# Performance work log

Hardware: AMD Instinct MI355X
Metric: run time of the kernel (lower is better)

Reference implementation:

```python
import jax, jax.numpy as jnp
import numpy as np

NEG_INF = -1e9


def _gru_cell(x, h, W_ih, W_hh, b_ih, b_hh):
    # torch GRUCell math, gate order [r; z; n]
    gx = x @ W_ih.T + b_ih          # [B, 3H]
    gh = h @ W_hh.T + b_hh          # [B, 3H]
    xr, xz, xn = jnp.split(gx, 3, axis=-1)
    hr, hz, hn = jnp.split(gh, 3, axis=-1)
    r = jax.nn.sigmoid(xr + hr)
    z = jax.nn.sigmoid(xz + hz)
    n = jnp.tanh(xn + r * hn)
    return (1.0 - z) * n + z * h


def setup_inputs() -> dict:
    key = jax.random.key(0)
    ks = jax.random.split(key, 8)
    B, N, D, H, P = 64, 2048, 256, 256, 256
    s = 0.05
    return {
        "sequence": jax.random.normal(ks[0], (B, N, D), jnp.float32),
        "hidden_t": jax.random.normal(ks[1], (B, H), jnp.float32),
        "sequence_mask": jnp.ones((B, N), jnp.float32),
        "num_steps": 2,
        "W_seq": jax.random.normal(ks[2], (D, P), jnp.float32) * s,
        "W_h": jax.random.normal(ks[3], (H, P), jnp.float32) * s,
        "v_att": jax.random.normal(ks[4], (P,), jnp.float32) * s,
        "W_ih": jax.random.normal(ks[5], (3 * H, D), jnp.float32) * s,
        "W_hh": jax.random.normal(ks[6], (3 * H, H), jnp.float32) * s,
        "b_ih": jnp.zeros((3 * H,), jnp.float32),
        "b_hh": jnp.zeros((3 * H,), jnp.float32),
    }


def reference(sequence, hidden_t, sequence_mask, num_steps,
              W_seq, W_h, v_att, W_ih, W_hh, b_ih, b_hh):
    # Precompute the sequence projection once (invariant across decode steps).
    seq_proj = jnp.einsum("bnd,dp->bnp", sequence, W_seq)   # [B, N, P]
    mask_bias = jnp.where(sequence_mask > 0, 0.0, NEG_INF)  # [B, N]

    def step(h, _):
        # projection similarity: v . tanh(W1 s_i + W2 h)
        proj = jnp.tanh(seq_proj + (h @ W_h)[:, None, :])   # [B, N, P]
        scores = jnp.einsum("bnp,p->bn", proj, v_att) + mask_bias
        w = jax.nn.softmax(scores, axis=-1)                  # [B, N]
        vec = jnp.einsum("bn,bnd->bd", w, sequence)          # [B, D]
        h_new = _gru_cell(vec, h, W_ih, W_hh, b_ih, b_hh)
        return h_new, w

    _, ws = jax.lax.scan(step, hidden_t, None, length=num_steps)  # [T, B, N]
    return jnp.transpose(ws, (1, 0, 2))                            # [B, T, N]
```

## Files before the change

### kernel.cpp

```cpp
#include <hip/hip_runtime.h>
#include <cstdint>

using u16 = unsigned short;
using u32 = unsigned int;
typedef __attribute__((ext_vector_type(8))) short bf16x8;
typedef __attribute__((ext_vector_type(8))) u16 u16x8;
typedef __attribute__((ext_vector_type(16))) float f32x16;
typedef __attribute__((ext_vector_type(4))) u32 u32x4;

#define DEV static __device__ __forceinline__

DEV u16 bf16_rne(float x) {
  u32 u = __float_as_uint(x);
  u32 r = (u + 0x7FFFu + ((u >> 16) & 1u)) >> 16;
  return (u16)r;
}
DEV float bf16f(u16 h) { return __uint_as_float(((u32)h) << 16); }

DEV u32 cvt_pk_bf16(float lo, float hi) {
  u32 d;
  asm("v_cvt_pk_bf16_f32 %0, %1, %2" : "=v"(d) : "v"(lo), "v"(hi));
  return d;
}

DEV float fast_tanh(float x) {
  float e = __expf(2.0f * x);
  return 1.0f - 2.0f / (e + 1.0f);
}
DEV float sigmoidf_(float x) { return 1.0f / (1.0f + __expf(-x)); }

__global__ __launch_bounds__(256) void prep_w(const float* __restrict__ Wseq,
                                              const float* __restrict__ Wih,
                                              const float* __restrict__ Whh,
                                              u16* __restrict__ WfG,
                                              float* __restrict__ WT,
                                              float* __restrict__ UT) {
  const int bid = blockIdx.x, t = threadIdx.x;
  if (bid < 32) {
    const int unit = bid * 4 + (t >> 6);
    const int lane = t & 63, l31 = lane & 31, koct = lane >> 5;
    const int pt8 = unit >> 4, kt = unit & 15;
    u16x8 o;
#pragma unroll
    for (int e = 0; e < 8; ++e)
      o[e] = bf16_rne(
          Wseq[(long)(kt * 16 + koct * 8 + e) * 256 + pt8 * 32 + l31]);
    *(u16x8*)(WfG + (long)unit * 512 + lane * 8) = o;
  } else {
    const int gid = bid - 32;
    const float* src = (gid >= 12) ? Whh : Wih;
    float* dst = (gid >= 12) ? UT : WT;
    const int g = (gid % 12) * 64 + (t & 63);
    const int dq = t >> 6;
#pragma unroll 4
    for (int d = dq * 64; d < dq * 64 + 64; ++d)
      dst[(long)d * 768 + g] = src[(long)g * 256 + d];
  }
}

__global__ __launch_bounds__(256) void hw_q(const float* __restrict__ h,
                                            const float* __restrict__ Wh,
                                            float* __restrict__ hw) {
  const int q = blockIdx.x, b = blockIdx.y, t = threadIdx.x;
  __shared__ float sh[256];
  __shared__ float sP[4][64];
  sh[t] = h[b * 256 + t];
  __syncthreads();
  const int j4 = t & 63, dg = t >> 6;
  const int j = q * 64 + j4;
  float g = 0.f;
#pragma unroll 4
  for (int k = dg * 64; k < dg * 64 + 64; ++k)
    g = fmaf(sh[k], Wh[(long)k * 256 + j], g);
  sP[dg][j4] = g;
  __syncthreads();
  if (t < 64)
    hw[b * 256 + q * 64 + t] = (sP[0][t] + sP[1][t]) + (sP[2][t] + sP[3][t]);
}

struct EpiSmem {
  float sQ[64][5];
  float se[64];
  float shw[256];
  float svv[256];
};

DEV void epilogue(EpiSmem& sm, const f32x16& a00, const f32x16& a10,
                  const u16* bs, const float* __restrict__ mask,
                  float* __restrict__ wbuf, float* __restrict__ esum,
                  float* __restrict__ part, long nbase, int esumIdx,
                  long partBase, int t, int lane, int w, int l31, int koct,
                  int pg, int ng) {
  float sc0 = 0.f;
#pragma unroll
  for (int r = 0; r < 16; ++r) {
    const int pidx = pg * 64 + (r & 3) + 8 * (r >> 2) + 4 * koct;
    sc0 = fmaf(sm.svv[pidx], fast_tanh(a00[r] + sm.shw[pidx]), sc0);
  }
#pragma unroll
  for (int r = 0; r < 16; ++r) {
    const int pidx = pg * 64 + 32 + (r & 3) + 8 * (r >> 2) + 4 * koct;
    sc0 = fmaf(sm.svv[pidx], fast_tanh(a10[r] + sm.shw[pidx]), sc0);
  }
  sc0 += __shfl_xor(sc0, 32, 64);
  if (koct == 0) sm.sQ[ng * 32 + l31][pg] = sc0;
  __syncthreads();
  if (t < 64) {
    float s = (sm.sQ[t][0] + sm.sQ[t][1]) + (sm.sQ[t][2] + sm.sQ[t][3]);
    const long n = nbase + t;
    float e = (mask[n] > 0.f) ? __expf(s) : 0.f;
    sm.se[t] = e;
    wbuf[n] = e;
    float s4 = e;
#pragma unroll
    for (int off = 1; off < 64; off <<= 1) s4 += __shfl_xor(s4, off, 64);
    if (t == 0) esum[esumIdx] = s4;
  }
  __syncthreads();
#pragma unroll
  for (int kk = 0; kk < 2; ++kk) {
    const int kt = w + kk * 8;
    float vd0 = 0, vd1 = 0, vd2 = 0, vd3 = 0, vd4 = 0, vd5 = 0, vd6 = 0,
          vd7 = 0;
#pragma unroll
    for (int t8 = 0; t8 < 2; ++t8) {
      u16x8 q = *(const u16x8*)(bs + ((long)(t8 * 16 + kt) * 64 + lane) * 8);
      const float wv = sm.se[t8 * 32 + l31];
      vd0 = fmaf(wv, bf16f((u16)q[0]), vd0);
      vd1 = fmaf(wv, bf16f((u16)q[1]), vd1);
      vd2 = fmaf(wv, bf16f((u16)q[2]), vd2);
      vd3 = fmaf(wv, bf16f((u16)q[3]), vd3);
      vd4 = fmaf(wv, bf16f((u16)q[4]), vd4);
      vd5 = fmaf(wv, bf16f((u16)q[5]), vd5);
      vd6 = fmaf(wv, bf16f((u16)q[6]), vd6);
      vd7 = fmaf(wv, bf16f((u16)q[7]), vd7);
    }
#pragma unroll
    for (int off = 1; off < 32; off <<= 1) {
      vd0 += __shfl_xor(vd0, off, 64);
      vd1 += __shfl_xor(vd1, off, 64);
      vd2 += __shfl_xor(vd2, off, 64);
      vd3 += __shfl_xor(vd3, off, 64);
      vd4 += __shfl_xor(vd4, off, 64);
      vd5 += __shfl_xor(vd5, off, 64);
      vd6 += __shfl_xor(vd6, off, 64);
      vd7 += __shfl_xor(vd7, off, 64);
    }
    if (l31 == 0) {
      float4 o0 = {vd0, vd1, vd2, vd3};
      float4 o1 = {vd4, vd5, vd6, vd7};
      float* pp = part + partBase * 256 + kt * 16 + koct * 8;
      *(float4*)pp = o0;
      *(float4*)(pp + 4) = o1;
    }
  }
}

__global__ __launch_bounds__(512, 4) void step0k(
    const float* __restrict__ seq, u16* __restrict__ seqF,
    const u16* __restrict__ WfG, const float* __restrict__ hwbuf,
    const float* __restrict__ vatt, const float* __restrict__ mask,
    float* __restrict__ wbuf, float* __restrict__ esum,
    float* __restrict__ part, int N, int NCH, int B) {
  __shared__ __align__(16) u16 sR[16384];
  __shared__ EpiSmem sm;

  const int t = threadIdx.x, lane = t & 63, w = t >> 6;
  const int l31 = lane & 31, koct = lane >> 5;
  const int pg = w >> 1, ng = w & 1;
  const int b = blockIdx.y, ch = blockIdx.x;
  char* sRb = (char*)sR;
  const long chbase = (long)(b * NCH + ch) << 14;

  {
    const float* src = seq + ((long)b * N + ch * 64) * 256;
#pragma unroll
    for (int i = 0; i < 4; ++i) {
      const int idx = i * 4096 + t * 8;
      float4 x = *(const float4*)(src + idx);
      float4 y = *(const float4*)(src + idx + 4);
      u32x4 o;
      o[0] = cvt_pk_bf16(x.x, x.y);
      o[1] = cvt_pk_bf16(x.z, x.w);
      o[2] = cvt_pk_bf16(y.x, y.y);
      o[3] = cvt_pk_bf16(y.z, y.w);
      const int row = idx >> 8, colb = (idx & 255) * 2;
      *(u32x4*)(sRb + row * 512 + (colb ^ ((row & 31) << 4))) = o;
    }
  }
  if (t < 256) {
    sm.shw[t] = hwbuf[b * 256 + t];
    sm.svv[t] = vatt[t];
  }
  __syncthreads();

  {
    u16* dst = seqF + chbase;
#pragma unroll
    for (int i = 0; i < 4; ++i) {
      const int uidx = i * 512 + t;
      const int ln = uidx & 63, unit = uidx >> 6;
      const int kt = unit & 15, t8 = unit >> 4;
      const int row = t8 * 32 + (ln & 31);
      const int colb = (kt * 16 + (ln >> 5) * 8) * 2;
      u16x8 v = *(const u16x8*)(sRb + row * 512 + (colb ^ ((row & 31) << 4)));
      *(u16x8*)(dst + (long)uidx * 8) = v;
    }
  }

  f32x16 a00 = (f32x16)0.f, a10 = (f32x16)0.f;
  {
    const u16* wa0 = WfG + (long)pg * 16384 + lane * 8;
    const u16* wa1 = wa0 + 8192;
    const int row0 = ng * 32 + l31;
    const char* p0 = sRb + row0 * 512;
    const int sw0 = (row0 & 31) << 4;
    const int cb = koct * 16;
#pragma unroll 4
    for (int kt = 0; kt < 16; ++kt) {
      bf16x8 af0 = *(const bf16x8*)(wa0 + kt * 512);
      bf16x8 af1 = *(const bf16x8*)(wa1 + kt * 512);
      bf16x8 bf0 = *(const bf16x8*)(p0 + ((kt * 32 + cb) ^ sw0));
      a00 = __builtin_amdgcn_mfma_f32_32x32x16_bf16(af0, bf0, a00, 0, 0, 0);
      a10 = __builtin_amdgcn_mfma_f32_32x32x16_bf16(af1, bf0, a10, 0, 0, 0);
    }
  }
  __syncthreads();
  epilogue(sm, a00, a10, seqF + chbase, mask, wbuf, esum, part,
           (long)b * N + ch * 64, b * NCH + ch, (long)ch * B + b, t, lane, w,
           l31, koct, pg, ng);
}

__global__ __launch_bounds__(512, 4) void step1k(
    const u16* __restrict__ seqF, const u16* __restrict__ WfG,
    const float* __restrict__ hwbuf, const float* __restrict__ vatt,
    const float* __restrict__ mask, float* __restrict__ wbuf,
    float* __restrict__ esum, float* __restrict__ part, int N, int NCH,
    int B) {
  __shared__ EpiSmem sm;
  const int t = threadIdx.x, lane = t & 63, w = t >> 6;
  const int l31 = lane & 31, koct = lane >> 5;
  const int pg = w >> 1, ng = w & 1;
  const int b = blockIdx.y, ch = blockIdx.x;
  const long chbase = (long)(b * NCH + ch) << 14;

  if (t < 256) {
    sm.shw[t] = hwbuf[b * 256 + t];
    sm.svv[t] = vatt[t];
  }

  const u16* bs0 = seqF + chbase + ng * 8192 + lane * 8;
  const u16* wa0 = WfG + (long)pg * 16384 + lane * 8;
  const u16* wa1 = wa0 + 8192;

  f32x16 a00 = (f32x16)0.f, a10 = (f32x16)0.f;

  u16x8 A0c, A1c, B0c, A0n, A1n, B0n;
  A0c = *(const u16x8*)(wa0);
  A1c = *(const u16x8*)(wa1);
  B0c = *(const u16x8*)(bs0);

#define MFMA2(A0, A1, B0)                                                      \
  {                                                                            \
    bf16x8 af0 = *(bf16x8*)&A0, af1 = *(bf16x8*)&A1;                           \
    bf16x8 bf0 = *(bf16x8*)&B0;                                                \
    a00 = __builtin_amdgcn_mfma_f32_32x32x16_bf16(af0, bf0, a00, 0, 0, 0);     \
    a10 = __builtin_amdgcn_mfma_f32_32x32x16_bf16(af1, bf0, a10, 0, 0, 0);     \
  }

#pragma unroll
  for (int kt2 = 0; kt2 < 8; ++kt2) {
    const int kn = kt2 * 2 + 1;
    A0n = *(const u16x8*)(wa0 + kn * 512);
    A1n = *(const u16x8*)(wa1 + kn * 512);
    B0n = *(const u16x8*)(bs0 + kn * 512);
    MFMA2(A0c, A1c, B0c);
    if (kt2 < 7) {
      const int kc = kt2 * 2 + 2;
      A0c = *(const u16x8*)(wa0 + kc * 512);
      A1c = *(const u16x8*)(wa1 + kc * 512);
      B0c = *(const u16x8*)(bs0 + kc * 512);
    }
    MFMA2(A0n, A1n, B0n);
  }
#undef MFMA2

  __syncthreads();
  epilogue(sm, a00, a10, seqF + chbase, mask, wbuf, esum, part,
           (long)b * N + ch * 64, b * NCH + ch, (long)ch * B + b, t, lane, w,
           l31, koct, pg, ng);
}

__global__ __launch_bounds__(256) void finalize_gru(
    const float* __restrict__ part, const float* __restrict__ esumP, int ecnt,
    const float* __restrict__ hprev, const float* __restrict__ WT,
    const float* __restrict__ UT, const float* __restrict__ bih,
    const float* __restrict__ bhh, const float* __restrict__ wbuf,
    float* __restrict__ out, float* __restrict__ hnew, int N, int T, int step,
    int NP, int B) {
  const int q = blockIdx.x, b = blockIdx.y, t = threadIdx.x;
  __shared__ float sv[256], sh[256], sP[6][4][64];
  float S = 0.f;
  for (int i = 0; i < ecnt; ++i) S += esumP[b * ecnt + i];
  const float inv = 1.f / S;
  float a = 0.f;
  for (int cc = 0; cc < NP; ++cc) a += part[((long)cc * B + b) * 256 + t];
  sv[t] = a * inv;
  sh[t] = hprev[b * 256 + t];
  __syncthreads();
  const int j4 = t & 63, dg = t >> 6;
  const int j = q * 64 + j4;
  float g0 = 0, g1 = 0, g2 = 0, g3 = 0, g4 = 0, g5 = 0;
#pragma unroll 4
  for (int d = dg * 64; d < dg * 64 + 64; ++d) {
    const float vd = sv[d], hd = sh[d];
    const float* wr_ = WT + (long)d * 768 + j;
    const float* ur_ = UT + (long)d * 768 + j;
    g0 = fmaf(vd, wr_[0], g0);
    g1 = fmaf(vd, wr_[256], g1);
    g2 = fmaf(vd, wr_[512], g2);
    g3 = fmaf(hd, ur_[0], g3);
    g4 = fmaf(hd, ur_[256], g4);
    g5 = fmaf(hd, ur_[512], g5);
  }
  sP[0][dg][j4] = g0;
  sP[1][dg][j4] = g1;
  sP[2][dg][j4] = g2;
  sP[3][dg][j4] = g3;
  sP[4][dg][j4] = g4;
  sP[5][dg][j4] = g5;
  __syncthreads();
  if (t < 64) {
    const int jj = q * 64 + t;
    float xr = bih[jj], xz = bih[256 + jj], xn = bih[512 + jj];
    float hr = bhh[jj], hz = bhh[256 + jj], hn = bhh[512 + jj];
#pragma unroll
    for (int dgg = 0; dgg < 4; ++dgg) {
      xr += sP[0][dgg][t];
      xz += sP[1][dgg][t];
      xn += sP[2][dgg][t];
      hr += sP[3][dgg][t];
      hz += sP[4][dgg][t];
      hn += sP[5][dgg][t];
    }
    float rr = sigmoidf_(xr + hr);
    float zz = sigmoidf_(xz + hz);
    float nn = fast_tanh(xn + rr * hn);
    hnew[b * 256 + jj] = (1.f - zz) * nn + zz * sh[jj];
  }
  const long ob = ((long)b * T + step) * N;
  const int nq = N >> 2;
  for (int i = 0; i * 256 < nq; ++i) {
    const int n = q * nq + i * 256 + t;
    out[ob + n] = wbuf[(long)b * N + n] * inv;
  }
}

extern "C" void kernel_launch(void* const* d_in, const int* in_sizes, int n_in,
                              void* d_out, int out_size, void* d_ws,
                              size_t ws_size, hipStream_t stream) {
  (void)n_in;
  (void)ws_size;
  const float* seq = (const float*)d_in[0];
  const float* hidden = (const float*)d_in[1];
  const float* mask = (const float*)d_in[2];
  const float* Wseq = (const float*)d_in[4];
  const float* Wh = (const float*)d_in[5];
  const float* vatt = (const float*)d_in[6];
  const float* Wih = (const float*)d_in[7];
  const float* Whh = (const float*)d_in[8];
  const float* bih = (const float*)d_in[9];
  const float* bhh = (const float*)d_in[10];
  float* out = (float*)d_out;

  const int P = in_sizes[6];
  const int H = in_sizes[5] / P;
  const int B = in_sizes[1] / H;
  const int N = in_sizes[2] / B;
  const int T = out_size / (B * N);
  const long M = (long)B * N;
  const int NCH = N / 64;

  char* p = (char*)d_ws;
  auto alloc = [&](size_t bytes) {
    char* r = p;
    p += (bytes + 255) & ~(size_t)255;
    return r;
  };
  u16* seqF = (u16*)alloc((size_t)M * 256 * 2);
  u16* WfG = (u16*)alloc((size_t)256 * 256 * 2);
  float* WT = (float*)alloc((size_t)256 * 768 * 4);
  float* UT = (float*)alloc((size_t)256 * 768 * 4);
  float* wbuf = (float*)alloc((size_t)B * N * 4);
  float* hwbuf = (float*)alloc((size_t)B * 256 * 4);
  float* hA = (float*)alloc((size_t)B * 256 * 4);
  float* hB = (float*)alloc((size_t)B * 256 * 4);
  float* part = (float*)alloc((size_t)NCH * B * 256 * 4);
  float* esum = (float*)alloc((size_t)B * NCH * 4);
  float* hbuf[2] = {hA, hB};

  prep_w<<<dim3(56), dim3(256), 0, stream>>>(Wseq, Wih, Whh, WfG, WT, UT);

  for (int t = 0; t < T; ++t) {
    const float* hcur = (t == 0) ? hidden : hbuf[(t - 1) & 1];
    hw_q<<<dim3(4, B), dim3(256), 0, stream>>>(hcur, Wh, hwbuf);
    if (t == 0) {
      step0k<<<dim3(NCH, B), dim3(512), 0, stream>>>(
          seq, seqF, WfG, hwbuf, vatt, mask, wbuf, esum, part, N, NCH, B);
    } else {
      step1k<<<dim3(NCH, B), dim3(512), 0, stream>>>(
          seqF, WfG, hwbuf, vatt, mask, wbuf, esum, part, N, NCH, B);
    }
    finalize_gru<<<dim3(4, B), dim3(256), 0, stream>>>(
        part, esum, NCH, hcur, WT, UT, bih, bhh, wbuf, out, hbuf[t & 1], N, T,
        t, NCH, B);
  }
}
```

Baseline: 163.0 us.

## Split bf16 sequence conversion into separate prep kernel and unify step kernels

Moves the fp32-to-bf16 swizzled conversion of the sequence out of the first step kernel into a dedicated prep_seqF kernel, so every step runs the same register-pipelined stepk that reads seqF from global memory. Step 0 no longer uses a 32KB LDS tile, which may raise occupancy. The cost is an extra launch and a full write-then-read round trip of seqF in step 0. The epilogue score accumulation also changes from a serial FMA chain to a tree reduction over 32 partial products, which shortens the dependency chain but uses more registers.

```diff
diff --git a/kernel.cpp b/kernel.cpp
--- a/kernel.cpp
+++ b/kernel.cpp
@@ -58,6 +58,43 @@
   }
 }
 
+__global__ __launch_bounds__(512) void prep_seqF(const float* __restrict__ seq,
+                                                 u16* __restrict__ seqF, int N,
+                                                 int NCH) {
+  __shared__ __align__(16) u16 sR[16384];
+  const int t = threadIdx.x;
+  const int b = blockIdx.y, ch = blockIdx.x;
+  char* sRb = (char*)sR;
+  const long chbase = (long)(b * NCH + ch) << 14;
+
+  const float* src = seq + ((long)b * N + ch * 64) * 256;
+#pragma unroll
+  for (int i = 0; i < 4; ++i) {
+    const int idx = i * 4096 + t * 8;
+    float4 x = *(const float4*)(src + idx);
+    float4 y = *(const float4*)(src + idx + 4);
+    u32x4 o;
+    o[0] = cvt_pk_bf16(x.x, x.y);
+    o[1] = cvt_pk_bf16(x.z, x.w);
+    o[2] = cvt_pk_bf16(y.x, y.y);
+    o[3] = cvt_pk_bf16(y.z, y.w);
+    const int row = idx >> 8, colb = (idx & 255) * 2;
+    *(u32x4*)(sRb + row * 512 + (colb ^ ((row & 31) << 4))) = o;
+  }
+  __syncthreads();
+  u16* dst = seqF + chbase;
+#pragma unroll
+  for (int i = 0; i < 4; ++i) {
+    const int uidx = i * 512 + t;
+    const int ln = uidx & 63, unit = uidx >> 6;
+    const int kt = unit & 15, t8 = unit >> 4;
+    const int row = t8 * 32 + (ln & 31);
+    const int colb = (kt * 16 + (ln >> 5) * 8) * 2;
+    u16x8 v = *(const u16x8*)(sRb + row * 512 + (colb ^ ((row & 31) << 4)));
+    *(u16x8*)(dst + (long)uidx * 8) = v;
+  }
+}
+
 __global__ __launch_bounds__(256) void hw_q(const float* __restrict__ h,
                                             const float* __restrict__ Wh,
                                             float* __restrict__ hw) {
@@ -78,166 +115,16 @@
     hw[b * 256 + q * 64 + t] = (sP[0][t] + sP[1][t]) + (sP[2][t] + sP[3][t]);
 }
 
-struct EpiSmem {
-  float sQ[64][5];
-  float se[64];
-  float shw[256];
-  float svv[256];
-};
-
-DEV void epilogue(EpiSmem& sm, const f32x16& a00, const f32x16& a10,
-                  const u16* bs, const float* __restrict__ mask,
-                  float* __restrict__ wbuf, float* __restrict__ esum,
-                  float* __restrict__ part, long nbase, int esumIdx,
-                  long partBase, int t, int lane, int w, int l31, int koct,
-                  int pg, int ng) {
-  float sc0 = 0.f;
-#pragma unroll
-  for (int r = 0; r < 16; ++r) {
-    const int pidx = pg * 64 + (r & 3) + 8 * (r >> 2) + 4 * koct;
-    sc0 = fmaf(sm.svv[pidx], fast_tanh(a00[r] + sm.shw[pidx]), sc0);
-  }
-#pragma unroll
-  for (int r = 0; r < 16; ++r) {
-    const int pidx = pg * 64 + 32 + (r & 3) + 8 * (r >> 2) + 4 * koct;
-    sc0 = fmaf(sm.svv[pidx], fast_tanh(a10[r] + sm.shw[pidx]), sc0);
-  }
-  sc0 += __shfl_xor(sc0, 32, 64);
-  if (koct == 0) sm.sQ[ng * 32 + l31][pg] = sc0;
-  __syncthreads();
-  if (t < 64) {
-    float s = (sm.sQ[t][0] + sm.sQ[t][1]) + (sm.sQ[t][2] + sm.sQ[t][3]);
-    const long n = nbase + t;
-    float e = (mask[n] > 0.f) ? __expf(s) : 0.f;
-    sm.se[t] = e;
-    wbuf[n] = e;
-    float s4 = e;
-#pragma unroll
-    for (int off = 1; off < 64; off <<= 1) s4 += __shfl_xor(s4, off, 64);
-    if (t == 0) esum[esumIdx] = s4;
-  }
-  __syncthreads();
-#pragma unroll
-  for (int kk = 0; kk < 2; ++kk) {
-    const int kt = w + kk * 8;
-    float vd0 = 0, vd1 = 0, vd2 = 0, vd3 = 0, vd4 = 0, vd5 = 0, vd6 = 0,
-          vd7 = 0;
-#pragma unroll
-    for (int t8 = 0; t8 < 2; ++t8) {
-      u16x8 q = *(const u16x8*)(bs + ((long)(t8 * 16 + kt) * 64 + lane) * 8);
-      const float wv = sm.se[t8 * 32 + l31];
-      vd0 = fmaf(wv, bf16f((u16)q[0]), vd0);
-      vd1 = fmaf(wv, bf16f((u16)q[1]), vd1);
-      vd2 = fmaf(wv, bf16f((u16)q[2]), vd2);
-      vd3 = fmaf(wv, bf16f((u16)q[3]), vd3);
-      vd4 = fmaf(wv, bf16f((u16)q[4]), vd4);
-      vd5 = fmaf(wv, bf16f((u16)q[5]), vd5);
-      vd6 = fmaf(wv, bf16f((u16)q[6]), vd6);
-      vd7 = fmaf(wv, bf16f((u16)q[7]), vd7);
-    }
-#pragma unroll
-    for (int off = 1; off < 32; off <<= 1) {
-      vd0 += __shfl_xor(vd0, off, 64);
-      vd1 += __shfl_xor(vd1, off, 64);
-      vd2 += __shfl_xor(vd2, off, 64);
-      vd3 += __shfl_xor(vd3, off, 64);
-      vd4 += __shfl_xor(vd4, off, 64);
-      vd5 += __shfl_xor(vd5, off, 64);
-      vd6 += __shfl_xor(vd6, off, 64);
-      vd7 += __shfl_xor(vd7, off, 64);
-    }
-    if (l31 == 0) {
-      float4 o0 = {vd0, vd1, vd2, vd3};
-      float4 o1 = {vd4, vd5, vd6, vd7};
-      float* pp = part + partBase * 256 + kt * 16 + koct * 8;
-      *(float4*)pp = o0;
-      *(float4*)(pp + 4) = o1;
-    }
-  }
-}
-
-__global__ __launch_bounds__(512, 4) void step0k(
-    const float* __restrict__ seq, u16* __restrict__ seqF,
-    const u16* __restrict__ WfG, const float* __restrict__ hwbuf,
-    const float* __restrict__ vatt, const float* __restrict__ mask,
-    float* __restrict__ wbuf, float* __restrict__ esum,
-    float* __restrict__ part, int N, int NCH, int B) {
-  __shared__ __align__(16) u16 sR[16384];
-  __shared__ EpiSmem sm;
-
-  const int t = threadIdx.x, lane = t & 63, w = t >> 6;
-  const int l31 = lane & 31, koct = lane >> 5;
-  const int pg = w >> 1, ng = w & 1;
-  const int b = blockIdx.y, ch = blockIdx.x;
-  char* sRb = (char*)sR;
-  const long chbase = (long)(b * NCH + ch) << 14;
-
-  {
-    const float* src = seq + ((long)b * N + ch * 64) * 256;
-#pragma unroll
-    for (int i = 0; i < 4; ++i) {
-      const int idx = i * 4096 + t * 8;
-      float4 x = *(const float4*)(src + idx);
-      float4 y = *(const float4*)(src + idx + 4);
-      u32x4 o;
-      o[0] = cvt_pk_bf16(x.x, x.y);
-      o[1] = cvt_pk_bf16(x.z, x.w);
-      o[2] = cvt_pk_bf16(y.x, y.y);
-      o[3] = cvt_pk_bf16(y.z, y.w);
-      const int row = idx >> 8, colb = (idx & 255) * 2;
-      *(u32x4*)(sRb + row * 512 + (colb ^ ((row & 31) << 4))) = o;
-    }
-  }
-  if (t < 256) {
-    sm.shw[t] = hwbuf[b * 256 + t];
-    sm.svv[t] = vatt[t];
-  }
-  __syncthreads();
-
-  {
-    u16* dst = seqF + chbase;
-#pragma unroll
-    for (int i = 0; i < 4; ++i) {
-      const int uidx = i * 512 + t;
-      const int ln = uidx & 63, unit = uidx >> 6;
-      const int kt = unit & 15, t8 = unit >> 4;
-      const int row = t8 * 32 + (ln & 31);
-      const int colb = (kt * 16 + (ln >> 5) * 8) * 2;
-      u16x8 v = *(const u16x8*)(sRb + row * 512 + (colb ^ ((row & 31) << 4)));
-      *(u16x8*)(dst + (long)uidx * 8) = v;
-    }
-  }
-
-  f32x16 a00 = (f32x16)0.f, a10 = (f32x16)0.f;
-  {
-    const u16* wa0 = WfG + (long)pg * 16384 + lane * 8;
-    const u16* wa1 = wa0 + 8192;
-    const int row0 = ng * 32 + l31;
-    const char* p0 = sRb + row0 * 512;
-    const int sw0 = (row0 & 31) << 4;
-    const int cb = koct * 16;
-#pragma unroll 4
-    for (int kt = 0; kt < 16; ++kt) {
-      bf16x8 af0 = *(const bf16x8*)(wa0 + kt * 512);
-      bf16x8 af1 = *(const bf16x8*)(wa1 + kt * 512);
-      bf16x8 bf0 = *(const bf16x8*)(p0 + ((kt * 32 + cb) ^ sw0));
-      a00 = __builtin_amdgcn_mfma_f32_32x32x16_bf16(af0, bf0, a00, 0, 0, 0);
-      a10 = __builtin_amdgcn_mfma_f32_32x32x16_bf16(af1, bf0, a10, 0, 0, 0);
-    }
-  }
-  __syncthreads();
-  epilogue(sm, a00, a10, seqF + chbase, mask, wbuf, esum, part,
-           (long)b * N + ch * 64, b * NCH + ch, (long)ch * B + b, t, lane, w,
-           l31, koct, pg, ng);
-}
-
-__global__ __launch_bounds__(512, 4) void step1k(
+__global__ __launch_bounds__(512, 4) void stepk(
     const u16* __restrict__ seqF, const u16* __restrict__ WfG,
     const float* __restrict__ hwbuf, const float* __restrict__ vatt,
     const float* __restrict__ mask, float* __restrict__ wbuf,
     float* __restrict__ esum, float* __restrict__ part, int N, int NCH,
     int B) {
-  __shared__ EpiSmem sm;
+  __shared__ float sQ[64][5];
+  __shared__ float se[64];
+  __shared__ float shw[256], svv[256];
+
   const int t = threadIdx.x, lane = t & 63, w = t >> 6;
   const int l31 = lane & 31, koct = lane >> 5;
   const int pg = w >> 1, ng = w & 1;
@@ -245,8 +132,8 @@
   const long chbase = (long)(b * NCH + ch) << 14;
 
   if (t < 256) {
-    sm.shw[t] = hwbuf[b * 256 + t];
-    sm.svv[t] = vatt[t];
+    shw[t] = hwbuf[b * 256 + t];
+    svv[t] = vatt[t];
   }
 
   const u16* bs0 = seqF + chbase + ng * 8192 + lane * 8;
@@ -286,9 +173,77 @@
 #undef MFMA2
 
   __syncthreads();
-  epilogue(sm, a00, a10, seqF + chbase, mask, wbuf, esum, part,
-           (long)b * N + ch * 64, b * NCH + ch, (long)ch * B + b, t, lane, w,
-           l31, koct, pg, ng);
+
+  float pr[32];
+#pragma unroll
+  for (int r = 0; r < 16; ++r) {
+    const int pidx = pg * 64 + (r & 3) + 8 * (r >> 2) + 4 * koct;
+    pr[r] = svv[pidx] * fast_tanh(a00[r] + shw[pidx]);
+  }
+#pragma unroll
+  for (int r = 0; r < 16; ++r) {
+    const int pidx = pg * 64 + 32 + (r & 3) + 8 * (r >> 2) + 4 * koct;
+    pr[16 + r] = svv[pidx] * fast_tanh(a10[r] + shw[pidx]);
+  }
+#pragma unroll
+  for (int st = 16; st >= 1; st >>= 1)
+#pragma unroll
+    for (int i = 0; i < st; ++i) pr[i] += pr[i + st];
+  float sc0 = pr[0];
+  sc0 += __shfl_xor(sc0, 32, 64);
+  if (koct == 0) sQ[ng * 32 + l31][pg] = sc0;
+  __syncthreads();
+  if (t < 64) {
+    float s = (sQ[t][0] + sQ[t][1]) + (sQ[t][2] + sQ[t][3]);
+    const long n = (long)b * N + ch * 64 + t;
+    float e = (mask[n] > 0.f) ? __expf(s) : 0.f;
+    se[t] = e;
+    wbuf[n] = e;
+    float s4 = e;
+#pragma unroll
+    for (int off = 1; off < 64; off <<= 1) s4 += __shfl_xor(s4, off, 64);
+    if (t == 0) esum[b * NCH + ch] = s4;
+  }
+  __syncthreads();
+
+  const u16* bs = seqF + chbase;
+#pragma unroll
+  for (int kk = 0; kk < 2; ++kk) {
+    const int kt = w + kk * 8;
+    float vd0 = 0, vd1 = 0, vd2 = 0, vd3 = 0, vd4 = 0, vd5 = 0, vd6 = 0,
+          vd7 = 0;
+#pragma unroll
+    for (int t8 = 0; t8 < 2; ++t8) {
+      u16x8 q = *(const u16x8*)(bs + ((long)(t8 * 16 + kt) * 64 + lane) * 8);
+      const float wv = se[t8 * 32 + l31];
+      vd0 = fmaf(wv, bf16f((u16)q[0]), vd0);
+      vd1 = fmaf(wv, bf16f((u16)q[1]), vd1);
+      vd2 = fmaf(wv, bf16f((u16)q[2]), vd2);
+      vd3 = fmaf(wv, bf16f((u16)q[3]), vd3);
+      vd4 = fmaf(wv, bf16f((u16)q[4]), vd4);
+      vd5 = fmaf(wv, bf16f((u16)q[5]), vd5);
+      vd6 = fmaf(wv, bf16f((u16)q[6]), vd6);
+      vd7 = fmaf(wv, bf16f((u16)q[7]), vd7);
+    }
+#pragma unroll
+    for (int off = 1; off < 32; off <<= 1) {
+      vd0 += __shfl_xor(vd0, off, 64);
+      vd1 += __shfl_xor(vd1, off, 64);
+      vd2 += __shfl_xor(vd2, off, 64);
+      vd3 += __shfl_xor(vd3, off, 64);
+      vd4 += __shfl_xor(vd4, off, 64);
+      vd5 += __shfl_xor(vd5, off, 64);
+      vd6 += __shfl_xor(vd6, off, 64);
+      vd7 += __shfl_xor(vd7, off, 64);
+    }
+    if (l31 == 0) {
+      float4 o0 = {vd0, vd1, vd2, vd3};
+      float4 o1 = {vd4, vd5, vd6, vd7};
+      float* pp = part + ((long)ch * B + b) * 256 + kt * 16 + koct * 8;
+      *(float4*)pp = o0;
+      *(float4*)(pp + 4) = o1;
+    }
+  }
 }
 
 __global__ __launch_bounds__(256) void finalize_gru(
@@ -400,17 +355,13 @@
   float* hbuf[2] = {hA, hB};
 
   prep_w<<<dim3(56), dim3(256), 0, stream>>>(Wseq, Wih, Whh, WfG, WT, UT);
+  prep_seqF<<<dim3(NCH, B), dim3(512), 0, stream>>>(seq, seqF, N, NCH);
 
   for (int t = 0; t < T; ++t) {
     const float* hcur = (t == 0) ? hidden : hbuf[(t - 1) & 1];
     hw_q<<<dim3(4, B), dim3(256), 0, stream>>>(hcur, Wh, hwbuf);
-    if (t == 0) {
-      step0k<<<dim3(NCH, B), dim3(512), 0, stream>>>(
-          seq, seqF, WfG, hwbuf, vatt, mask, wbuf, esum, part, N, NCH, B);
-    } else {
-      step1k<<<dim3(NCH, B), dim3(512), 0, stream>>>(
-          seqF, WfG, hwbuf, vatt, mask, wbuf, esum, part, N, NCH, B);
-    }
+    stepk<<<dim3(NCH, B), dim3(512), 0, stream>>>(
+        seqF, WfG, hwbuf, vatt, mask, wbuf, esum, part, N, NCH, B);
     finalize_gru<<<dim3(4, B), dim3(256), 0, stream>>>(
         part, esum, NCH, hcur, WT, UT, bih, bhh, wbuf, out, hbuf[t & 1], N, T,
         t, NCH, B);
```

After: 180.2 us. 10.6% more time.
